# Optimization experiments

Hardware: AMD Instinct MI355X
Metric: run time of the kernel (lower is better)

## Reference

```python
import jax, jax.numpy as jnp
import numpy as np

N = 4_194_304   # collocation points
H = 10          # num_neurons
L = 10          # num_layers (residual blocks)
DIN = 3         # (x, y, z) coords
DOUT = 1        # traveltime


def _linear_params(k, fan_in, fan_out, batch=()):
    # matches torch.nn.Linear default init: U(-1/sqrt(fan_in), 1/sqrt(fan_in))
    kw, kb = jax.random.split(k)
    s = 1.0 / np.sqrt(fan_in)
    W = jax.random.uniform(kw, batch + (fan_in, fan_out), minval=-s, maxval=s, dtype=jnp.float32)
    b = jax.random.uniform(kb, batch + (fan_out,), minval=-s, maxval=s, dtype=jnp.float32)
    return W, b


def setup_inputs() -> dict:
    key = jax.random.key(0)
    ks = jax.random.split(key, 8)
    x = jax.random.normal(ks[0], (N, DIN), dtype=jnp.float32)
    w0, b0 = _linear_params(ks[1], DIN, H)
    w1, b1 = _linear_params(ks[2], H, H)
    Wr1, Br1 = _linear_params(ks[3], H, H, (L,))
    Wr2, Br2 = _linear_params(ks[4], H, H, (L,))
    Wr3, Br3 = _linear_params(ks[5], H, H, (L,))
    w8, b8 = _linear_params(ks[6], H, H)
    w9, b9 = _linear_params(ks[7], H, DOUT)
    return dict(x=x, w0=w0, b0=b0, w1=w1, b1=b1,
                Wr1=Wr1, Br1=Br1, Wr2=Wr2, Br2=Br2, Wr3=Wr3, Br3=Br3,
                w8=w8, b8=b8, w9=w9, b9=b9)


def reference(x, w0, b0, w1, b1, Wr1, Br1, Wr2, Br2, Wr3, Br3, w8, b8, w9, b9):
    relu = jax.nn.relu
    h = relu(x @ w0 + b0)          # [N, H]
    h = relu(h @ w1 + b1)          # [N, H]

    def block(h, params):
        W1, B1, W2, B2, W3, B3 = params
        h1 = relu(h @ W1 + B1)
        h2 = relu(h1 @ W3 + B3 + h @ W2 + B2)  # residual mixing of x0 via W2
        return h2, None

    h, _ = jax.lax.scan(block, h, (Wr1, Br1, Wr2, Br2, Wr3, Br3))
    h = relu(h @ w8 + b8)
    out = h @ w9 + b9              # last_act=None, last_abs=False, last_multiplier=1
    return out
```

## Files before the change

### kernel.cpp

```cpp
#include <hip/hip_runtime.h>


#define NPTS 4194304
#define NBLK 2048
#define WPB 4
#define NWAVES (NBLK * WPB)
#define NTILES (NPTS / 32)
#define TPW (NTILES / NWAVES)
#define NMM 24
#define ILP 4

typedef _Float16 h8 __attribute__((ext_vector_type(8)));
typedef float v16f __attribute__((ext_vector_type(16)));
typedef unsigned u4v __attribute__((ext_vector_type(4)));

#define PIN4(a) asm volatile("" : "+v"(a[0]), "+v"(a[1]), "+v"(a[2]), "+v"(a[3]))

__device__ __forceinline__ v16f mm(h8 a, h8 b, v16f c) {
    return __builtin_amdgcn_mfma_f32_32x32x16_f16(a, b, c, 0, 0, 0);
}
__device__ __forceinline__ unsigned pkrtz(float a, float b) {
    return __builtin_bit_cast(unsigned, __builtin_amdgcn_cvt_pkrtz(a, b));
}
__device__ __forceinline__ h8 relu8(h8 h) {
    h8 z = {0, 0, 0, 0, 0, 0, 0, 0};
    return __builtin_elementwise_max(h, z);
}
__device__ __forceinline__ h8 rc_lo(v16f d) {
    u4v u;
    u.x = pkrtz(d[0], d[1]); u.y = pkrtz(d[2], d[3]);
    u.z = pkrtz(d[4], d[5]); u.w = pkrtz(d[6], d[7]);
    return relu8(__builtin_bit_cast(h8, u));
}
__device__ __forceinline__ h8 rc_hi(v16f d) {
    u4v u;
    u.x = pkrtz(d[8], d[9]);   u.y = pkrtz(d[10], d[11]);
    u.z = pkrtz(d[12], d[13]); u.w = pkrtz(d[14], d[15]);
    return relu8(__builtin_bit_cast(h8, u));
}

__global__ __launch_bounds__(64) void prepack(
    const float* __restrict__ w0, const float* __restrict__ b0,
    const float* __restrict__ w1, const float* __restrict__ b1,
    const float* __restrict__ Wr1, const float* __restrict__ Br1,
    const float* __restrict__ Wr2, const float* __restrict__ Br2,
    const float* __restrict__ Wr3, const float* __restrict__ Br3,
    const float* __restrict__ w8, const float* __restrict__ b8,
    const float* __restrict__ w9, const float* __restrict__ b9,
    h8* __restrict__ tab)
{
    const int q = blockIdx.x, l = threadIdx.x;
    const int m = l & 31, g = l >> 5;
    h8 v;
#pragma unroll
    for (int j = 0; j < 8; ++j) {
        const int rr = (j & 3) + 8 * (j >> 2) + 4 * g;
        float a = 0.0f;
        if (q == 0) {
            if (m < 10 && rr < 3)        a = w0[rr * 10 + m];
            else if (m < 10 && rr == 3)  a = b0[m];
            else if (m == 10 && rr == 3) a = 1.0f;
        } else if (q == 1 || q == 22) {
            const float* W = (q == 1) ? w1 : w8;
            const float* B = (q == 1) ? b1 : b8;
            if (m < 10 && rr < 10)        a = W[rr * 10 + m];
            else if (m < 10 && rr == 10)  a = B[m];
            else if (m == 10 && rr == 10) a = 1.0f;
        } else if (q == 23) {
            if (m == 0 && rr < 10)       a = w9[rr];
            else if (m == 0 && rr == 10) a = b9[0];
        } else if (((q - 2) & 1) == 0) {
            const int bl = (q - 2) >> 1;
            if (m < 10) {
                if (rr < 10)       a = Wr1[bl * 100 + rr * 10 + m];
                else if (rr == 10) a = Br1[bl * 10 + m];
            } else if (m >= 16 && m < 26) {
                if (rr < 10)       a = Wr2[bl * 100 + rr * 10 + (m - 16)];
                else if (rr == 10) a = Br2[bl * 10 + (m - 16)] + Br3[bl * 10 + (m - 16)];
            } else if (m == 26 && rr == 10) {
                a = 1.0f;
            }
        } else {
            const int bl = (q - 3) >> 1;
            if (m >= 16 && m < 26 && rr < 10)
                a = Wr3[bl * 100 + rr * 10 + (m - 16)];
        }
        v[j] = (_Float16)a;
    }
    tab[q * 64 + l] = v;
}

__global__ __launch_bounds__(256, 4) void resnet_fwd(
    const float* __restrict__ x,
    const h8* __restrict__ tab,
    float* __restrict__ out)
{
    __shared__ h8 sA[NMM * 64];
    for (int i = threadIdx.x; i < NMM * 64; i += 256) sA[i] = tab[i];
    __syncthreads();

    const int lane = threadIdx.x & 63;
    const int wv = blockIdx.x * WPB + (threadIdx.x >> 6);
    const int col = lane & 31;
    const bool lo = lane < 32;

    v16f zero;
#pragma unroll
    for (int j = 0; j < 16; ++j) zero[j] = 0.0f;
    asm volatile("" : "+v"(zero));

    const long p0 = (long)wv * TPW * 32;
    const float* px = x + (p0 + col) * 3;
    float* po = out + p0 + col;

    for (int t = 0; t < TPW; t += ILP) {
        int ln = lane;
        asm volatile("" : "+v"(ln));
        const h8* wp = &sA[ln];

        h8 hh[ILP];
#pragma unroll
        for (int c = 0; c < ILP; ++c) {
            float a0 = 0.f, a1 = 0.f, a2 = 0.f;
            if (lo) { a0 = px[c * 96 + 0]; a1 = px[c * 96 + 1];
                      a2 = px[c * 96 + 2]; }
            u4v u;
            u.x = pkrtz(a0, a1); u.y = pkrtz(a2, lo ? 1.0f : 0.0f);
            u.z = 0u; u.w = 0u;
            hh[c] = __builtin_bit_cast(h8, u);
        }
        PIN4(hh);

        {
            h8 a0 = wp[0 * 64];
#pragma unroll
            for (int c = 0; c < ILP; ++c) hh[c] = rc_lo(mm(a0, hh[c], zero));
            PIN4(hh);
            h8 a1 = wp[1 * 64];
#pragma unroll
            for (int c = 0; c < ILP; ++c) hh[c] = rc_lo(mm(a1, hh[c], zero));
            PIN4(hh);
        }

#pragma unroll
        for (int bl = 0; bl < 10; ++bl) {
            h8 a12 = wp[(2 + 2 * bl) * 64];
            h8 a3  = wp[(3 + 2 * bl) * 64];
            v16f d12[ILP];
#pragma unroll
            for (int c = 0; c < ILP; ++c) d12[c] = mm(a12, hh[c], zero);
            PIN4(d12);
#pragma unroll
            for (int c = 0; c < ILP; ++c) {
                h8 t1 = rc_lo(d12[c]);
                d12[c] = mm(a3, t1, d12[c]);
            }
            PIN4(d12);
#pragma unroll
            for (int c = 0; c < ILP; ++c) hh[c] = rc_hi(d12[c]);
            PIN4(hh);
        }

        {
            h8 a8 = wp[22 * 64];
#pragma unroll
            for (int c = 0; c < ILP; ++c) hh[c] = rc_lo(mm(a8, hh[c], zero));
            PIN4(hh);
        }

        {
            h8 a9 = wp[23 * 64];
#pragma unroll
            for (int c = 0; c < ILP; ++c) {
                v16f d = mm(a9, hh[c], zero);
                if (lo) po[c * 32] = d[0];
            }
        }

        px += ILP * 96;
        po += ILP * 32;
    }
}

extern "C" void kernel_launch(void* const* d_in, const int* in_sizes, int n_in,
                              void* d_out, int out_size, void* d_ws, size_t ws_size,
                              hipStream_t stream)
{
    const float* x   = (const float*)d_in[0];
    const float* w0  = (const float*)d_in[1];
    const float* b0  = (const float*)d_in[2];
    const float* w1  = (const float*)d_in[3];
    const float* b1  = (const float*)d_in[4];
    const float* Wr1 = (const float*)d_in[5];
    const float* Br1 = (const float*)d_in[6];
    const float* Wr2 = (const float*)d_in[7];
    const float* Br2 = (const float*)d_in[8];
    const float* Wr3 = (const float*)d_in[9];
    const float* Br3 = (const float*)d_in[10];
    const float* w8  = (const float*)d_in[11];
    const float* b8  = (const float*)d_in[12];
    const float* w9  = (const float*)d_in[13];
    const float* b9  = (const float*)d_in[14];
    float* out = (float*)d_out;
    h8* tab = (h8*)d_ws;

    hipLaunchKernelGGL(prepack, dim3(NMM), dim3(64), 0, stream,
                       w0, b0, w1, b1, Wr1, Br1, Wr2, Br2, Wr3, Br3,
                       w8, b8, w9, b9, tab);

    hipLaunchKernelGGL(resnet_fwd, dim3(NBLK), dim3(256), 0, stream,
                       x, (const h8*)tab, out);
}
```

Before: 176.5 us.

## Halve per-wave ILP and impose MFMA/VALU schedule groups

Cuts the number of independent 32-point tiles in flight per wave from four to two. The asm register pins are replaced with sched_group_barrier hints that group MFMA and VALU work into phases. The x loads are now unconditional, with a select applied afterwards instead of a branch. The aim is lower register pressure and a cleaner MFMA/convert schedule, at the cost of less latency hiding within each wave.

```diff
diff --git a/kernel.cpp b/kernel.cpp
--- a/kernel.cpp
+++ b/kernel.cpp
@@ -8,13 +8,14 @@
 #define NTILES (NPTS / 32)
 #define TPW (NTILES / NWAVES)
 #define NMM 24
-#define ILP 4
+#define ILP 2
 
 typedef _Float16 h8 __attribute__((ext_vector_type(8)));
 typedef float v16f __attribute__((ext_vector_type(16)));
 typedef unsigned u4v __attribute__((ext_vector_type(4)));
 
-#define PIN4(a) asm volatile("" : "+v"(a[0]), "+v"(a[1]), "+v"(a[2]), "+v"(a[3]))
+#define SGB_MFMA(n) __builtin_amdgcn_sched_group_barrier(0x8, n, 0)
+#define SGB_VALU(n) __builtin_amdgcn_sched_group_barrier(0x2, n, 0)
 
 __device__ __forceinline__ v16f mm(h8 a, h8 b, v16f c) {
     return __builtin_amdgcn_mfma_f32_32x32x16_f16(a, b, c, 0, 0, 0);
@@ -121,25 +122,37 @@
         h8 hh[ILP];
 #pragma unroll
         for (int c = 0; c < ILP; ++c) {
-            float a0 = 0.f, a1 = 0.f, a2 = 0.f;
-            if (lo) { a0 = px[c * 96 + 0]; a1 = px[c * 96 + 1];
-                      a2 = px[c * 96 + 2]; }
+            float a0 = px[c * 96 + 0];
+            float a1 = px[c * 96 + 1];
+            float a2 = px[c * 96 + 2];
+            a0 = lo ? a0 : 0.0f;
+            a1 = lo ? a1 : 0.0f;
+            a2 = lo ? a2 : 0.0f;
             u4v u;
             u.x = pkrtz(a0, a1); u.y = pkrtz(a2, lo ? 1.0f : 0.0f);
             u.z = 0u; u.w = 0u;
             hh[c] = __builtin_bit_cast(h8, u);
         }
-        PIN4(hh);
 
         {
             h8 a0 = wp[0 * 64];
-#pragma unroll
-            for (int c = 0; c < ILP; ++c) hh[c] = rc_lo(mm(a0, hh[c], zero));
-            PIN4(hh);
+            v16f d[ILP];
+#pragma unroll
+            for (int c = 0; c < ILP; ++c) d[c] = mm(a0, hh[c], zero);
+            SGB_MFMA(2);
+#pragma unroll
+            for (int c = 0; c < ILP; ++c) hh[c] = rc_lo(d[c]);
+            SGB_VALU(16);
+        }
+        {
             h8 a1 = wp[1 * 64];
-#pragma unroll
-            for (int c = 0; c < ILP; ++c) hh[c] = rc_lo(mm(a1, hh[c], zero));
-            PIN4(hh);
+            v16f d[ILP];
+#pragma unroll
+            for (int c = 0; c < ILP; ++c) d[c] = mm(a1, hh[c], zero);
+            SGB_MFMA(2);
+#pragma unroll
+            for (int c = 0; c < ILP; ++c) hh[c] = rc_lo(d[c]);
+            SGB_VALU(16);
         }
 
 #pragma unroll
@@ -149,32 +162,39 @@
             v16f d12[ILP];
 #pragma unroll
             for (int c = 0; c < ILP; ++c) d12[c] = mm(a12, hh[c], zero);
-            PIN4(d12);
-#pragma unroll
-            for (int c = 0; c < ILP; ++c) {
-                h8 t1 = rc_lo(d12[c]);
-                d12[c] = mm(a3, t1, d12[c]);
-            }
-            PIN4(d12);
+            SGB_MFMA(2);
+            h8 t1[ILP];
+#pragma unroll
+            for (int c = 0; c < ILP; ++c) t1[c] = rc_lo(d12[c]);
+            SGB_VALU(16);
+#pragma unroll
+            for (int c = 0; c < ILP; ++c) d12[c] = mm(a3, t1[c], d12[c]);
+            SGB_MFMA(2);
 #pragma unroll
             for (int c = 0; c < ILP; ++c) hh[c] = rc_hi(d12[c]);
-            PIN4(hh);
+            SGB_VALU(16);
         }
 
         {
             h8 a8 = wp[22 * 64];
-#pragma unroll
-            for (int c = 0; c < ILP; ++c) hh[c] = rc_lo(mm(a8, hh[c], zero));
-            PIN4(hh);
+            v16f d[ILP];
+#pragma unroll
+            for (int c = 0; c < ILP; ++c) d[c] = mm(a8, hh[c], zero);
+            SGB_MFMA(2);
+#pragma unroll
+            for (int c = 0; c < ILP; ++c) hh[c] = rc_lo(d[c]);
+            SGB_VALU(16);
         }
 
         {
             h8 a9 = wp[23 * 64];
-#pragma unroll
-            for (int c = 0; c < ILP; ++c) {
-                v16f d = mm(a9, hh[c], zero);
-                if (lo) po[c * 32] = d[0];
-            }
+            v16f d[ILP];
+#pragma unroll
+            for (int c = 0; c < ILP; ++c) d[c] = mm(a9, hh[c], zero);
+            SGB_MFMA(2);
+#pragma unroll
+            for (int c = 0; c < ILP; ++c)
+                if (lo) po[c * 32] = d[c][0];
         }
 
         px += ILP * 96;
```

After: 173.6 us (median of 2 runs). No clear change (-1.7%).

## Hand-schedule MFMA chain in inline asm with LDS weight prefetch and input prefetch

Applied to the files above, without the earlier changes.

Replaces the compiler-generated MFMA chain with one inline assembly block over fixed VGPRs. It double-buffers the weight fragments from LDS via ds_read while the MFMAs execute and inserts explicit s_nop hazard padding. It halves per-wave ILP from 4 to 2 tiles and prefetches the next iteration's x coordinates into registers. The aim is to cut compiler scheduling overhead and VGPR pressure, at the cost of less latency hiding per wave. Fixed register clobbers and hard-coded nop counts also add correctness and hazard risk.

```diff
diff --git a/kernel.cpp b/kernel.cpp
--- a/kernel.cpp
+++ b/kernel.cpp
@@ -8,35 +8,14 @@
 #define NTILES (NPTS / 32)
 #define TPW (NTILES / NWAVES)
 #define NMM 24
-#define ILP 4
+#define ILP 2
 
 typedef _Float16 h8 __attribute__((ext_vector_type(8)));
 typedef float v16f __attribute__((ext_vector_type(16)));
 typedef unsigned u4v __attribute__((ext_vector_type(4)));
 
-#define PIN4(a) asm volatile("" : "+v"(a[0]), "+v"(a[1]), "+v"(a[2]), "+v"(a[3]))
-
-__device__ __forceinline__ v16f mm(h8 a, h8 b, v16f c) {
-    return __builtin_amdgcn_mfma_f32_32x32x16_f16(a, b, c, 0, 0, 0);
-}
 __device__ __forceinline__ unsigned pkrtz(float a, float b) {
     return __builtin_bit_cast(unsigned, __builtin_amdgcn_cvt_pkrtz(a, b));
-}
-__device__ __forceinline__ h8 relu8(h8 h) {
-    h8 z = {0, 0, 0, 0, 0, 0, 0, 0};
-    return __builtin_elementwise_max(h, z);
-}
-__device__ __forceinline__ h8 rc_lo(v16f d) {
-    u4v u;
-    u.x = pkrtz(d[0], d[1]); u.y = pkrtz(d[2], d[3]);
-    u.z = pkrtz(d[4], d[5]); u.w = pkrtz(d[6], d[7]);
-    return relu8(__builtin_bit_cast(h8, u));
-}
-__device__ __forceinline__ h8 rc_hi(v16f d) {
-    u4v u;
-    u.x = pkrtz(d[8], d[9]);   u.y = pkrtz(d[10], d[11]);
-    u.z = pkrtz(d[12], d[13]); u.w = pkrtz(d[14], d[15]);
-    return relu8(__builtin_bit_cast(h8, u));
 }
 
 __global__ __launch_bounds__(64) void prepack(
@@ -90,6 +69,127 @@
     tab[q * 64 + l] = v;
 }
 
+#define MM(D, A, B, C) "v_mfma_f32_32x32x16_f16 " D ", " A ", " B ", " C "\n"
+#define CVT(T, S0, S1) "v_cvt_pkrtz_f16_f32 " T ", " S0 ", " S1 "\n"
+#define PKM(T)         "v_pk_max_f16 " T ", " T ", 0\n"
+#define NOP19          "s_nop 7\ns_nop 7\ns_nop 2\n"
+#define NOP2           "s_nop 1\n"
+
+#define SD0  "v[48:63]"
+#define SD1  "v[64:79]"
+#define SZ   "v[80:95]"
+#define ST10 "v[96:99]"
+#define ST11 "v[100:103]"
+#define A12A "v[104:107]"
+#define A3A  "v[108:111]"
+#define A12B "v[112:115]"
+#define A3B  "v[116:119]"
+#define SH0  "v[120:123]"
+#define SH1  "v[124:127]"
+
+#define RC_LO_D0(T0,T1,T2,T3) \
+    CVT(T0,"v48","v49") CVT(T1,"v50","v51") CVT(T2,"v52","v53") CVT(T3,"v54","v55") \
+    PKM(T0) PKM(T1) PKM(T2) PKM(T3)
+#define RC_LO_D1(T0,T1,T2,T3) \
+    CVT(T0,"v64","v65") CVT(T1,"v66","v67") CVT(T2,"v68","v69") CVT(T3,"v70","v71") \
+    PKM(T0) PKM(T1) PKM(T2) PKM(T3)
+#define RC_HI_D0(T0,T1,T2,T3) \
+    CVT(T0,"v56","v57") CVT(T1,"v58","v59") CVT(T2,"v60","v61") CVT(T3,"v62","v63") \
+    PKM(T0) PKM(T1) PKM(T2) PKM(T3)
+#define RC_HI_D1(T0,T1,T2,T3) \
+    CVT(T0,"v72","v73") CVT(T1,"v74","v75") CVT(T2,"v76","v77") CVT(T3,"v78","v79") \
+    PKM(T0) PKM(T1) PKM(T2) PKM(T3)
+
+#define PAIR_BLOCK(A12, A3, PF0, PF1, PD0, PD1) \
+    "s_waitcnt lgkmcnt(2)\n" \
+    MM(SD0, A12, SH0, SZ) \
+    MM(SD1, A12, SH1, SZ) \
+    NOP19 \
+    RC_LO_D0("v96","v97","v98","v99") \
+    RC_LO_D1("v100","v101","v102","v103") \
+    NOP2 \
+    MM(SD0, A3, ST10, SD0) \
+    MM(SD1, A3, ST11, SD1) \
+    "ds_read_b128 " PD0 ", %[ad] offset:" PF0 "\n" \
+    "ds_read_b128 " PD1 ", %[ad] offset:" PF1 "\n" \
+    "s_nop 7\ns_nop 7\ns_nop 1\n" \
+    RC_HI_D0("v120","v121","v122","v123") \
+    RC_HI_D1("v124","v125","v126","v127") \
+    NOP2
+
+#define PAIR_FIRST \
+    "s_waitcnt lgkmcnt(2)\n" \
+    MM(SD0, A12A, SH0, SZ) \
+    MM(SD1, A12A, SH1, SZ) \
+    NOP19 \
+    RC_LO_D0("v120","v121","v122","v123") \
+    RC_LO_D1("v124","v125","v126","v127") \
+    NOP2 \
+    MM(SD0, A3A, SH0, SZ) \
+    MM(SD1, A3A, SH1, SZ) \
+    "ds_read_b128 " A12A ", %[ad] offset:4096\n" \
+    "ds_read_b128 " A3A ", %[ad] offset:5120\n" \
+    "s_nop 7\ns_nop 7\ns_nop 1\n" \
+    RC_LO_D0("v120","v121","v122","v123") \
+    RC_LO_D1("v124","v125","v126","v127") \
+    NOP2
+
+#define PAIR_LAST \
+    "s_waitcnt lgkmcnt(2)\n" \
+    MM(SD0, A12B, SH0, SZ) \
+    MM(SD1, A12B, SH1, SZ) \
+    NOP19 \
+    RC_LO_D0("v120","v121","v122","v123") \
+    RC_LO_D1("v124","v125","v126","v127") \
+    NOP2 \
+    MM(SD0, A3B, SH0, SZ) \
+    MM(SD1, A3B, SH1, SZ) \
+    NOP19 \
+    "s_waitcnt lgkmcnt(0)\n" \
+    "v_mov_b32 %[o0], v48\n" \
+    "v_mov_b32 %[o1], v64\n"
+
+#define PROLOG \
+    "v_mov_b32 v80, 0\n"  "v_mov_b32 v81, 0\n"  "v_mov_b32 v82, 0\n"  "v_mov_b32 v83, 0\n" \
+    "v_mov_b32 v84, 0\n"  "v_mov_b32 v85, 0\n"  "v_mov_b32 v86, 0\n"  "v_mov_b32 v87, 0\n" \
+    "v_mov_b32 v88, 0\n"  "v_mov_b32 v89, 0\n"  "v_mov_b32 v90, 0\n"  "v_mov_b32 v91, 0\n" \
+    "v_mov_b32 v92, 0\n"  "v_mov_b32 v93, 0\n"  "v_mov_b32 v94, 0\n"  "v_mov_b32 v95, 0\n" \
+    "v_mov_b32 v120, %[h00]\n" "v_mov_b32 v121, %[h01]\n" \
+    "v_mov_b32 v122, 0\n"      "v_mov_b32 v123, 0\n" \
+    "v_mov_b32 v124, %[h10]\n" "v_mov_b32 v125, %[h11]\n" \
+    "v_mov_b32 v126, 0\n"      "v_mov_b32 v127, 0\n" \
+    "ds_read_b128 " A12A ", %[ad] offset:0\n" \
+    "ds_read_b128 " A3A  ", %[ad] offset:1024\n" \
+    "ds_read_b128 " A12B ", %[ad] offset:2048\n" \
+    "ds_read_b128 " A3B  ", %[ad] offset:3072\n"
+
+#define CHAIN_ASM \
+    PROLOG \
+    PAIR_FIRST \
+    PAIR_BLOCK(A12B, A3B,  "6144",  "7168", A12B, A3B) \
+    PAIR_BLOCK(A12A, A3A,  "8192",  "9216", A12A, A3A) \
+    PAIR_BLOCK(A12B, A3B, "10240", "11264", A12B, A3B) \
+    PAIR_BLOCK(A12A, A3A, "12288", "13312", A12A, A3A) \
+    PAIR_BLOCK(A12B, A3B, "14336", "15360", A12B, A3B) \
+    PAIR_BLOCK(A12A, A3A, "16384", "17408", A12A, A3A) \
+    PAIR_BLOCK(A12B, A3B, "18432", "19456", A12B, A3B) \
+    PAIR_BLOCK(A12A, A3A, "20480", "21504", A12A, A3A) \
+    PAIR_BLOCK(A12B, A3B, "22528", "23552", A12B, A3B) \
+    PAIR_BLOCK(A12A, A3A,     "0",     "0", A12A, A3A) \
+    PAIR_LAST
+
+#define VCLOB \
+    "v48","v49","v50","v51","v52","v53","v54","v55", \
+    "v56","v57","v58","v59","v60","v61","v62","v63", \
+    "v64","v65","v66","v67","v68","v69","v70","v71", \
+    "v72","v73","v74","v75","v76","v77","v78","v79", \
+    "v80","v81","v82","v83","v84","v85","v86","v87", \
+    "v88","v89","v90","v91","v92","v93","v94","v95", \
+    "v96","v97","v98","v99","v100","v101","v102","v103", \
+    "v104","v105","v106","v107","v108","v109","v110","v111", \
+    "v112","v113","v114","v115","v116","v117","v118","v119", \
+    "v120","v121","v122","v123","v124","v125","v126","v127"
+
 __global__ __launch_bounds__(256, 4) void resnet_fwd(
     const float* __restrict__ x,
     const h8* __restrict__ tab,
@@ -104,80 +204,52 @@
     const int col = lane & 31;
     const bool lo = lane < 32;
 
-    v16f zero;
-#pragma unroll
-    for (int j = 0; j < 16; ++j) zero[j] = 0.0f;
-    asm volatile("" : "+v"(zero));
+    const unsigned ad = (unsigned)(size_t)(&sA[lane]);
 
     const long p0 = (long)wv * TPW * 32;
     const float* px = x + (p0 + col) * 3;
     float* po = out + p0 + col;
 
+    float xa[ILP][3];
+#pragma unroll
+    for (int c = 0; c < ILP; ++c) {
+        xa[c][0] = px[c * 96 + 0]; xa[c][1] = px[c * 96 + 1];
+        xa[c][2] = px[c * 96 + 2];
+    }
+
+#pragma unroll 1
     for (int t = 0; t < TPW; t += ILP) {
-        int ln = lane;
-        asm volatile("" : "+v"(ln));
-        const h8* wp = &sA[ln];
-
-        h8 hh[ILP];
-#pragma unroll
-        for (int c = 0; c < ILP; ++c) {
-            float a0 = 0.f, a1 = 0.f, a2 = 0.f;
-            if (lo) { a0 = px[c * 96 + 0]; a1 = px[c * 96 + 1];
-                      a2 = px[c * 96 + 2]; }
-            u4v u;
-            u.x = pkrtz(a0, a1); u.y = pkrtz(a2, lo ? 1.0f : 0.0f);
-            u.z = 0u; u.w = 0u;
-            hh[c] = __builtin_bit_cast(h8, u);
+        unsigned h00, h01, h10, h11;
+        {
+            float a0 = lo ? xa[0][0] : 0.f, a1 = lo ? xa[0][1] : 0.f;
+            float a2 = lo ? xa[0][2] : 0.f;
+            h00 = pkrtz(a0, a1); h01 = pkrtz(a2, lo ? 1.0f : 0.0f);
+            float b0_ = lo ? xa[1][0] : 0.f, b1_ = lo ? xa[1][1] : 0.f;
+            float b2_ = lo ? xa[1][2] : 0.f;
+            h10 = pkrtz(b0_, b1_); h11 = pkrtz(b2_, lo ? 1.0f : 0.0f);
         }
-        PIN4(hh);
-
-        {
-            h8 a0 = wp[0 * 64];
-#pragma unroll
-            for (int c = 0; c < ILP; ++c) hh[c] = rc_lo(mm(a0, hh[c], zero));
-            PIN4(hh);
-            h8 a1 = wp[1 * 64];
-#pragma unroll
-            for (int c = 0; c < ILP; ++c) hh[c] = rc_lo(mm(a1, hh[c], zero));
-            PIN4(hh);
-        }
-
-#pragma unroll
-        for (int bl = 0; bl < 10; ++bl) {
-            h8 a12 = wp[(2 + 2 * bl) * 64];
-            h8 a3  = wp[(3 + 2 * bl) * 64];
-            v16f d12[ILP];
-#pragma unroll
-            for (int c = 0; c < ILP; ++c) d12[c] = mm(a12, hh[c], zero);
-            PIN4(d12);
+
+        const float* pn = px + ILP * 96;
+        if (t + ILP < TPW) {
 #pragma unroll
             for (int c = 0; c < ILP; ++c) {
-                h8 t1 = rc_lo(d12[c]);
-                d12[c] = mm(a3, t1, d12[c]);
-            }
-            PIN4(d12);
-#pragma unroll
-            for (int c = 0; c < ILP; ++c) hh[c] = rc_hi(d12[c]);
-            PIN4(hh);
-        }
-
-        {
-            h8 a8 = wp[22 * 64];
-#pragma unroll
-            for (int c = 0; c < ILP; ++c) hh[c] = rc_lo(mm(a8, hh[c], zero));
-            PIN4(hh);
-        }
-
-        {
-            h8 a9 = wp[23 * 64];
-#pragma unroll
-            for (int c = 0; c < ILP; ++c) {
-                v16f d = mm(a9, hh[c], zero);
-                if (lo) po[c * 32] = d[0];
+                xa[c][0] = pn[c * 96 + 0]; xa[c][1] = pn[c * 96 + 1];
+                xa[c][2] = pn[c * 96 + 2];
             }
         }
 
-        px += ILP * 96;
+        float o0, o1;
+        asm volatile(
+            CHAIN_ASM
+            : [o0] "=v"(o0), [o1] "=v"(o1)
+            : [h00] "v"(h00), [h01] "v"(h01),
+              [h10] "v"(h10), [h11] "v"(h11),
+              [ad] "v"(ad)
+            : VCLOB);
+
+        if (lo) { po[0] = o0; po[32] = o1; }
+
+        px = pn;
         po += ILP * 32;
     }
 }
```

Measured after the change: 179.5 us. No clear change (+1.7%).

## Halve ILP, raise occupancy, keep edge-layer weights in registers

Applied to the files above, without the earlier changes.

Cuts per-wave interleaving from 4 to 2 tiles, raises the launch-bounds occupancy hint from 4 to 6 blocks per CU, and drops the asm register-pinning barriers. The first, second and last two layer weight fragments are now held in registers for the whole kernel, while only the 20 residual-block fragments stay in LDS. The aim is to hide MFMA dependency latency through more resident waves instead of in-wave ILP. Each wave then has fewer independent MFMA chains, and without the pins the compiler may reschedule or spill.

```diff
diff --git a/kernel.cpp b/kernel.cpp
--- a/kernel.cpp
+++ b/kernel.cpp
@@ -8,13 +8,12 @@
 #define NTILES (NPTS / 32)
 #define TPW (NTILES / NWAVES)
 #define NMM 24
-#define ILP 4
+#define NLDS 20
+#define ILP 2
 
 typedef _Float16 h8 __attribute__((ext_vector_type(8)));
 typedef float v16f __attribute__((ext_vector_type(16)));
 typedef unsigned u4v __attribute__((ext_vector_type(4)));
-
-#define PIN4(a) asm volatile("" : "+v"(a[0]), "+v"(a[1]), "+v"(a[2]), "+v"(a[3]))
 
 __device__ __forceinline__ v16f mm(h8 a, h8 b, v16f c) {
     return __builtin_amdgcn_mfma_f32_32x32x16_f16(a, b, c, 0, 0, 0);
@@ -90,19 +89,24 @@
     tab[q * 64 + l] = v;
 }
 
-__global__ __launch_bounds__(256, 4) void resnet_fwd(
+__global__ __launch_bounds__(256, 6) void resnet_fwd(
     const float* __restrict__ x,
     const h8* __restrict__ tab,
     float* __restrict__ out)
 {
-    __shared__ h8 sA[NMM * 64];
-    for (int i = threadIdx.x; i < NMM * 64; i += 256) sA[i] = tab[i];
-    __syncthreads();
-
     const int lane = threadIdx.x & 63;
     const int wv = blockIdx.x * WPB + (threadIdx.x >> 6);
     const int col = lane & 31;
     const bool lo = lane < 32;
+
+    const h8 rA0 = tab[0 * 64 + lane];
+    const h8 rA1 = tab[1 * 64 + lane];
+    const h8 rA8 = tab[22 * 64 + lane];
+    const h8 rA9 = tab[23 * 64 + lane];
+
+    __shared__ h8 sA[NLDS * 64];
+    for (int i = threadIdx.x; i < NLDS * 64; i += 256) sA[i] = tab[128 + i];
+    __syncthreads();
 
     v16f zero;
 #pragma unroll
@@ -129,52 +133,35 @@
             u.z = 0u; u.w = 0u;
             hh[c] = __builtin_bit_cast(h8, u);
         }
-        PIN4(hh);
-
-        {
-            h8 a0 = wp[0 * 64];
-#pragma unroll
-            for (int c = 0; c < ILP; ++c) hh[c] = rc_lo(mm(a0, hh[c], zero));
-            PIN4(hh);
-            h8 a1 = wp[1 * 64];
-#pragma unroll
-            for (int c = 0; c < ILP; ++c) hh[c] = rc_lo(mm(a1, hh[c], zero));
-            PIN4(hh);
-        }
+
+#pragma unroll
+        for (int c = 0; c < ILP; ++c) hh[c] = rc_lo(mm(rA0, hh[c], zero));
+#pragma unroll
+        for (int c = 0; c < ILP; ++c) hh[c] = rc_lo(mm(rA1, hh[c], zero));
 
 #pragma unroll
         for (int bl = 0; bl < 10; ++bl) {
-            h8 a12 = wp[(2 + 2 * bl) * 64];
-            h8 a3  = wp[(3 + 2 * bl) * 64];
+            h8 a12 = wp[(2 * bl) * 64];
+            h8 a3  = wp[(2 * bl + 1) * 64];
             v16f d12[ILP];
 #pragma unroll
             for (int c = 0; c < ILP; ++c) d12[c] = mm(a12, hh[c], zero);
-            PIN4(d12);
 #pragma unroll
             for (int c = 0; c < ILP; ++c) {
                 h8 t1 = rc_lo(d12[c]);
                 d12[c] = mm(a3, t1, d12[c]);
             }
-            PIN4(d12);
 #pragma unroll
             for (int c = 0; c < ILP; ++c) hh[c] = rc_hi(d12[c]);
-            PIN4(hh);
-        }
-
-        {
-            h8 a8 = wp[22 * 64];
-#pragma unroll
-            for (int c = 0; c < ILP; ++c) hh[c] = rc_lo(mm(a8, hh[c], zero));
-            PIN4(hh);
-        }
-
-        {
-            h8 a9 = wp[23 * 64];
-#pragma unroll
-            for (int c = 0; c < ILP; ++c) {
-                v16f d = mm(a9, hh[c], zero);
-                if (lo) po[c * 32] = d[0];
-            }
+        }
+
+#pragma unroll
+        for (int c = 0; c < ILP; ++c) hh[c] = rc_lo(mm(rA8, hh[c], zero));
+
+#pragma unroll
+        for (int c = 0; c < ILP; ++c) {
+            v16f d = mm(rA9, hh[c], zero);
+            if (lo) po[c * 32] = d[0];
         }
 
         px += ILP * 96;
```

After: 174.2 us. No clear change (-1.3%).
